# Optimization experiments

Hardware: AMD Instinct MI355X
Metric: run time of the kernel (lower is better)

## Reference

```python
import jax, jax.numpy as jnp
import numpy as np

jax.config.update("jax_enable_x64", True)  # torch path computes in float64

MAX_BIT = 31
ACT_BIT = 8


def setup_inputs() -> dict:
    key = jax.random.key(0)
    k1, k2, k3, k4 = jax.random.split(key, 4)
    B, S, D = 8, 4096, 768
    x = jax.random.normal(k1, (B, S, D), dtype=jnp.float32)
    identity = jax.random.normal(k2, (B, S, D), dtype=jnp.float32)
    pre_act_scaling_factor = jax.random.uniform(k3, (D,), jnp.float32, 1e-3, 1e-2)
    identity_scaling_factor = jax.random.uniform(k4, (D,), jnp.float32, 1e-3, 1e-2)
    return {
        "x": x,
        "pre_act_scaling_factor": pre_act_scaling_factor,
        "identity": identity,
        "identity_scaling_factor": identity_scaling_factor,
    }


def _batch_frexp(v):
    # v > 0 (ratios of positive scales). frexp: v = m * 2**e with m in [0.5, 1).
    m, e = jnp.frexp(v.astype(jnp.float64))
    # Decimal ROUND_HALF_UP of m * 2**31 (m positive -> floor(x + 0.5))
    m_int = jnp.floor(m * (2.0 ** MAX_BIT) + 0.5)
    e_out = jnp.asarray(MAX_BIT, jnp.float64) - e.astype(jnp.float64)
    return m_int, e_out


def reference(x, pre_act_scaling_factor, identity, identity_scaling_factor):
    n = 2 ** (ACT_BIT - 1) - 1  # 127

    # ----- running-stat range tracking (min_val == max_val == 0 initially) -----
    x_act = x + identity
    min_val = x_act.min()
    max_val = x_act.max()
    eps = jnp.finfo(jnp.float32).eps
    z_scale = jnp.maximum(jnp.maximum(-min_val, max_val) / float(n), eps)  # scalar

    # ----- fixedpoint_mul (symmetric, bit_num=8) -----
    pre = pre_act_scaling_factor.reshape(1, 1, -1)   # [1,1,D]
    ids = identity_scaling_factor.reshape(1, 1, -1)  # [1,1,D]

    z_int = jnp.round(x / pre)  # banker's rounding, matches torch.round
    m, e = _batch_frexp(pre.astype(jnp.float64) / z_scale.astype(jnp.float64))
    output = jnp.round(z_int.astype(jnp.float64) * m / (2.0 ** e))

    wx_int = jnp.round(identity / ids)
    m1, e1 = _batch_frexp(ids.astype(jnp.float64) / z_scale.astype(jnp.float64))
    output1 = jnp.round(wx_int.astype(jnp.float64) * m1 / (2.0 ** e1))

    quant_int = jnp.clip((output + output1).astype(jnp.float32), -n - 1, n)

    out = quant_int * z_scale.astype(jnp.float32)
    return out, z_scale.reshape(1)
```

## Files before the change

kernel.cpp:

```cpp
#include <hip/hip_runtime.h>
#include <math.h>

static constexpr int kD = 768;
static constexpr int kRows = 32768;
static constexpr long long kN = (long long)kRows * kD;
static constexpr int kColGroups = 192;

static constexpr int kAmaxBlocks = 4096;
static constexpr int kQuantBlocks = 4096;
static constexpr int kQuantRows = 8;

typedef float nf4 __attribute__((ext_vector_type(4)));

__device__ __forceinline__ int swz(int bid, int nblk) {
    return (bid & 7) * (nblk >> 3) + (bid >> 3);
}

__global__ __launch_bounds__(256) void amax_kernel(
    const float4* __restrict__ x, const float4* __restrict__ idn,
    float* __restrict__ partial)
{
    const int b = swz((int)blockIdx.x, kAmaxBlocks);
    const int wave = threadIdx.x >> 6;
    const int lane = threadIdx.x & 63;
    const int base = (b * 4 + wave) * 384 + lane;

    float4 m4 = make_float4(0.f, 0.f, 0.f, 0.f);
    #pragma unroll
    for (int half = 0; half < 2; ++half) {
        const int o = base + half * 192;
        float4 a[3], c[3];
        #pragma unroll
        for (int j = 0; j < 3; ++j) a[j] = x[o + j * 64];
        #pragma unroll
        for (int j = 0; j < 3; ++j) c[j] = idn[o + j * 64];
        #pragma unroll
        for (int j = 0; j < 3; ++j) {
            m4.x = fmaxf(m4.x, fabsf(a[j].x + c[j].x));
            m4.y = fmaxf(m4.y, fabsf(a[j].y + c[j].y));
            m4.z = fmaxf(m4.z, fabsf(a[j].z + c[j].z));
            m4.w = fmaxf(m4.w, fabsf(a[j].w + c[j].w));
        }
    }
    float m = fmaxf(fmaxf(m4.x, m4.y), fmaxf(m4.z, m4.w));
    #pragma unroll
    for (int off = 32; off > 0; off >>= 1)
        m = fmaxf(m, __shfl_down(m, off, 64));

    __shared__ float wmax[4];
    if (lane == 0) wmax[wave] = m;
    __syncthreads();
    if (threadIdx.x == 0)
        partial[blockIdx.x] =
            fmaxf(fmaxf(wmax[0], wmax[1]), fmaxf(wmax[2], wmax[3]));
}

__device__ inline double quant_factor(double r) {
    int e;
    double mm = frexp(r, &e);
    double m_int = floor(mm * 2147483648.0 + 0.5);
    return ldexp(m_int, e - 31);
}

__global__ __launch_bounds__(768) void factor_kernel(
    const float* __restrict__ pre, const float* __restrict__ ids,
    const float* __restrict__ partial,
    double* __restrict__ fp, double* __restrict__ fi,
    float* __restrict__ z_scale_ws, float* __restrict__ out_scale)
{
    const int t = threadIdx.x;

    float m = 0.f;
    #pragma unroll
    for (int i = t; i < kAmaxBlocks; i += 768) m = fmaxf(m, partial[i]);
    #pragma unroll
    for (int off = 32; off > 0; off >>= 1)
        m = fmaxf(m, __shfl_down(m, off, 64));

    __shared__ float wmax[12];
    __shared__ float zs_sh;
    if ((t & 63) == 0) wmax[t >> 6] = m;
    __syncthreads();
    if (t == 0) {
        float mm = wmax[0];
        #pragma unroll
        for (int w = 1; w < 12; ++w) mm = fmaxf(mm, wmax[w]);
        float zs = fmaxf(mm / 127.0f, 1.1920928955078125e-07f);
        zs_sh = zs;
        *z_scale_ws = zs;
        *out_scale = zs;
    }
    __syncthreads();

    const double zsd = (double)zs_sh;
    if (t < kD) {
        fp[t] = quant_factor((double)pre[t] / zsd);
        fi[t] = quant_factor((double)ids[t] / zsd);
    }
}

__device__ inline float requant_elem(float xx, float ii, float p, float s,
                                     double fp, double fi, float z_scale) {
    float z_int = rintf(xx / p);
    float w_int = rintf(ii / s);
    double o  = rint((double)z_int * fp);
    double o1 = rint((double)w_int * fi);
    float q = (float)(o + o1);
    q = fminf(fmaxf(q, -128.0f), 127.0f);
    return q * z_scale;
}

template <int R>
__device__ __forceinline__ void quant_rows(
    const float4* __restrict__ x, const float4* __restrict__ idn,
    nf4* __restrict__ out, int rb,
    const float4& pf, const float4& sf,
    const double* fp, const double* fi, float z_scale)
{
    float4 xa[R], ia[R];
    #pragma unroll
    for (int j = 0; j < R; ++j) xa[j] = x[rb + j * kColGroups];
    #pragma unroll
    for (int j = 0; j < R; ++j) ia[j] = idn[rb + j * kColGroups];
    #pragma unroll
    for (int j = 0; j < R; ++j) {
        nf4 ov;
        ov.x = requant_elem(xa[j].x, ia[j].x, pf.x, sf.x, fp[0], fi[0], z_scale);
        ov.y = requant_elem(xa[j].y, ia[j].y, pf.y, sf.y, fp[1], fi[1], z_scale);
        ov.z = requant_elem(xa[j].z, ia[j].z, pf.z, sf.z, fp[2], fi[2], z_scale);
        ov.w = requant_elem(xa[j].w, ia[j].w, pf.w, sf.w, fp[3], fi[3], z_scale);
        __builtin_nontemporal_store(ov, &out[rb + j * kColGroups]);
    }
}

__global__ __launch_bounds__(192) void quant_kernel(
    const float4* __restrict__ x, const float4* __restrict__ idn,
    const float4* __restrict__ pre, const float4* __restrict__ ids,
    const float* __restrict__ z_scale_ws,
    const double* __restrict__ fp_tab, const double* __restrict__ fi_tab,
    nf4* __restrict__ out)
{
    const float z_scale = *z_scale_ws;

    const int b = swz((int)blockIdx.x, kQuantBlocks);
    const int t = threadIdx.x;
    const int base = b * (kQuantRows * kColGroups) + t;

    const float4 pf = pre[t];
    const float4 sf = ids[t];
    double fp[4], fi[4];
    #pragma unroll
    for (int j = 0; j < 4; ++j) { fp[j] = fp_tab[4*t + j]; fi[j] = fi_tab[4*t + j]; }

    quant_rows<3>(x, idn, out, base + 0 * kColGroups, pf, sf, fp, fi, z_scale);
    quant_rows<3>(x, idn, out, base + 3 * kColGroups, pf, sf, fp, fi, z_scale);
    quant_rows<2>(x, idn, out, base + 6 * kColGroups, pf, sf, fp, fi, z_scale);
}

extern "C" void kernel_launch(void* const* d_in, const int* in_sizes, int n_in,
                              void* d_out, int out_size, void* d_ws, size_t ws_size,
                              hipStream_t stream) {
    const float* x   = (const float*)d_in[0];
    const float* pre = (const float*)d_in[1];
    const float* idn = (const float*)d_in[2];
    const float* ids = (const float*)d_in[3];
    float* out = (float*)d_out;

    float* z_scale_ws = (float*)d_ws;
    float* partial = (float*)((char*)d_ws + 64);
    double* fp_tab = (double*)((char*)d_ws + 64 + kAmaxBlocks * sizeof(float));
    double* fi_tab = fp_tab + kD;

    amax_kernel<<<kAmaxBlocks, 256, 0, stream>>>(
        (const float4*)x, (const float4*)idn, partial);
    factor_kernel<<<1, 768, 0, stream>>>(pre, ids, partial, fp_tab, fi_tab,
                                         z_scale_ws, out + kN);
    quant_kernel<<<kQuantBlocks, 192, 0, stream>>>(
        (const float4*)x, (const float4*)idn,
        (const float4*)pre, (const float4*)ids,
        z_scale_ws, fp_tab, fi_tab, (nf4*)out);
}
```

Before: 281.1 us.

## Double-buffer amax loads through LDS with direct global-to-LDS copies

The amax reduction kernel now stages x and identity tiles into shared memory via global_load_lds with a two-stage double buffer. Each block handles twice as much data, so the block count is halved. The aim is to keep more loads in flight and overlap memory latency with the max computation. In exchange it adds barriers, LDS traffic, and hand-written vmcnt waits that must match the number of issued loads.

```diff
diff --git a/kernel.cpp b/kernel.cpp
--- a/kernel.cpp
+++ b/kernel.cpp
@@ -6,7 +6,7 @@
 static constexpr long long kN = (long long)kRows * kD;
 static constexpr int kColGroups = 192;
 
-static constexpr int kAmaxBlocks = 4096;
+static constexpr int kAmaxBlocks = 2048;
 static constexpr int kQuantBlocks = 4096;
 static constexpr int kQuantRows = 8;
 
@@ -15,33 +15,64 @@
 __device__ __forceinline__ int swz(int bid, int nblk) {
     return (bid & 7) * (nblk >> 3) + (bid >> 3);
 }
+
+__device__ __forceinline__ void gld16(const void* g, void* l) {
+    __builtin_amdgcn_global_load_lds(
+        (const __attribute__((address_space(1))) unsigned int*)g,
+        (__attribute__((address_space(3))) unsigned int*)l, 16, 0, 0);
+}
+
+#define WAITV(n) asm volatile("s_waitcnt vmcnt(" #n ")" ::: "memory")
+#define BARRIER() do { asm volatile("" ::: "memory"); \
+    __builtin_amdgcn_s_barrier(); asm volatile("" ::: "memory"); } while (0)
 
 __global__ __launch_bounds__(256) void amax_kernel(
     const float4* __restrict__ x, const float4* __restrict__ idn,
     float* __restrict__ partial)
 {
+    __shared__ float4 lx[2][512];
+    __shared__ float4 li[2][512];
+
     const int b = swz((int)blockIdx.x, kAmaxBlocks);
-    const int wave = threadIdx.x >> 6;
-    const int lane = threadIdx.x & 63;
-    const int base = (b * 4 + wave) * 384 + lane;
+    const int tid = threadIdx.x;
+    const int wave = tid >> 6;
+    const int lane = tid & 63;
+    const int gb = b * 3072;
+
+    auto issue = [&](int s, int buf) {
+        const int o = s * 512 + wave * 128;
+        #pragma unroll
+        for (int k = 0; k < 2; ++k)
+            gld16(&x[gb + o + k * 64 + lane], &lx[buf][wave * 128 + k * 64]);
+        #pragma unroll
+        for (int k = 0; k < 2; ++k)
+            gld16(&idn[gb + o + k * 64 + lane], &li[buf][wave * 128 + k * 64]);
+    };
 
     float4 m4 = make_float4(0.f, 0.f, 0.f, 0.f);
-    #pragma unroll
-    for (int half = 0; half < 2; ++half) {
-        const int o = base + half * 192;
-        float4 a[3], c[3];
-        #pragma unroll
-        for (int j = 0; j < 3; ++j) a[j] = x[o + j * 64];
-        #pragma unroll
-        for (int j = 0; j < 3; ++j) c[j] = idn[o + j * 64];
-        #pragma unroll
-        for (int j = 0; j < 3; ++j) {
-            m4.x = fmaxf(m4.x, fabsf(a[j].x + c[j].x));
-            m4.y = fmaxf(m4.y, fabsf(a[j].y + c[j].y));
-            m4.z = fmaxf(m4.z, fabsf(a[j].z + c[j].z));
-            m4.w = fmaxf(m4.w, fabsf(a[j].w + c[j].w));
+    auto compute = [&](int buf) {
+        #pragma unroll
+        for (int k = 0; k < 2; ++k) {
+            float4 a = lx[buf][k * 256 + tid];
+            float4 c = li[buf][k * 256 + tid];
+            m4.x = fmaxf(m4.x, fabsf(a.x + c.x));
+            m4.y = fmaxf(m4.y, fabsf(a.y + c.y));
+            m4.z = fmaxf(m4.z, fabsf(a.z + c.z));
+            m4.w = fmaxf(m4.w, fabsf(a.w + c.w));
         }
-    }
+    };
+
+    issue(0, 0);
+    issue(1, 1);
+    #pragma unroll 1
+    for (int s = 0; s < 6; ++s) {
+        if (s < 5) { WAITV(4); } else { WAITV(0); }
+        BARRIER();
+        compute(s & 1);
+        BARRIER();
+        if (s + 2 < 6) issue(s + 2, s & 1);
+    }
+
     float m = fmaxf(fmaxf(m4.x, m4.y), fmaxf(m4.z, m4.w));
     #pragma unroll
     for (int off = 32; off > 0; off >>= 1)
@@ -50,7 +81,7 @@
     __shared__ float wmax[4];
     if (lane == 0) wmax[wave] = m;
     __syncthreads();
-    if (threadIdx.x == 0)
+    if (tid == 0)
         partial[blockIdx.x] =
             fmaxf(fmaxf(wmax[0], wmax[1]), fmaxf(wmax[2], wmax[3]));
 }
```

Measured after the change: 286.6 us. Within noise of the previous version (+1.9%).
